# Kernel tuning notes

Measured on AMD Instinct MI355X. Metric: run time of the kernel, lower is better.

Reference implementation:

```python
import jax, jax.numpy as jnp
import numpy as np
from jax import lax


def conv2d(x, w, b=None, pad=0):
    out = lax.conv_general_dilated(x, w, (1, 1), [(pad, pad), (pad, pad)],
                                   dimension_numbers=('NCHW', 'OIHW', 'NCHW'))
    return out if b is None else out + b[None, :, None, None]


def bn_inf(x, gamma, beta, mean, var, eps=1e-5):
    inv = gamma / jnp.sqrt(var + eps)
    return x * inv[None, :, None, None] + (beta - mean * inv)[None, :, None, None]


def silu(x):
    return x * jax.nn.sigmoid(x)


def deform_conv2d(x, offset, weight, groups):
    # torchvision DeformConv2d v1 semantics: kernel 3x3, stride 1, pad 1, dilation 1,
    # one offset group; offset channels interleaved (dy, dx) per kernel tap, row-major taps.
    B, C, H, W = x.shape
    K = 9
    off = offset.reshape(B, K, 2, H, W)
    dy, dx = off[:, :, 0], off[:, :, 1]                      # (B,K,H,W)
    ki = (jnp.arange(K) // 3 - 1).astype(x.dtype)            # kernel row offset (pad=1)
    kj = (jnp.arange(K) % 3 - 1).astype(x.dtype)
    py = jnp.arange(H, dtype=x.dtype)[None, None, :, None] + ki[None, :, None, None] + dy
    px = jnp.arange(W, dtype=x.dtype)[None, None, None, :] + kj[None, :, None, None] + dx
    y0 = jnp.floor(py)
    x0 = jnp.floor(px)
    wy1 = py - y0                                            # bilinear weights
    wx1 = px - x0
    y0i = y0.astype(jnp.int32)
    x0i = x0.astype(jnp.int32)
    xf = x.reshape(B, C, H * W)

    def gather(yi, xi):
        valid = ((yi >= 0) & (yi < H) & (xi >= 0) & (xi < W)).astype(x.dtype)
        idx = (jnp.clip(yi, 0, H - 1) * W + jnp.clip(xi, 0, W - 1)).reshape(B, K * H * W)
        v = jax.vmap(lambda f, i: jnp.take(f, i, axis=-1))(xf, idx).reshape(B, C, K, H, W)
        return v * valid[:, None]

    cols = (gather(y0i, x0i) * ((1 - wy1) * (1 - wx1))[:, None]
            + gather(y0i, x0i + 1) * ((1 - wy1) * wx1)[:, None]
            + gather(y0i + 1, x0i) * (wy1 * (1 - wx1))[:, None]
            + gather(y0i + 1, x0i + 1) * (wy1 * wx1)[:, None])   # (B,C,K,H,W)

    G = groups
    Cg = C // G
    Co = weight.shape[0]
    cols = cols.reshape(B, G, Cg, K, H, W)
    wg = weight.reshape(G, Co // G, Cg, K)
    return jnp.einsum('bgckhw,gock->bgohw', cols, wg).reshape(B, Co, H, W)


def d_clem_forward(x, x_prev, w_off, b_off, w_def, w_cross, w_g1, b_g1,
                   g1_gamma, g1_beta, g1_mean, g1_var, w_g2, b_g2,
                   w_out, b_out, o_gamma, o_beta, o_mean, o_var):
    offset = conv2d(x, w_off, b_off, pad=1)
    x_dir = deform_conv2d(x, offset, w_def, groups=4)
    x_dense = conv2d(jnp.concatenate([x_dir, x_prev], axis=1), w_cross, None, pad=0)
    a = silu(bn_inf(conv2d(x_dense, w_g1, b_g1, pad=1), g1_gamma, g1_beta, g1_mean, g1_var))
    attn = jax.nn.sigmoid(conv2d(a, w_g2, b_g2, pad=0))
    out = silu(bn_inf(conv2d(x_dense * attn, w_out, b_out, pad=0), o_gamma, o_beta, o_mean, o_var))
    return x + out  # use_residual: in_channels == out_channels


def setup_inputs() -> dict:
    key = jax.random.key(0)
    ks = jax.random.split(key, 16)
    B, C, H, W, G = 4, 256, 64, 64, 4

    def wt(k, shape, fan_in):
        return jax.random.normal(k, shape, jnp.float32) / np.float32(np.sqrt(fan_in))

    return {
        'x': jax.random.normal(ks[0], (B, C, H, W), jnp.float32),
        'x_prev': jax.random.normal(ks[1], (B, C, H, W), jnp.float32),
        'w_off': wt(ks[2], (18, C, 3, 3), C * 9),
        'b_off': 0.01 * jax.random.normal(ks[3], (18,), jnp.float32),
        'w_def': wt(ks[4], (C, C // G, 3, 3), (C // G) * 9),
        'w_cross': wt(ks[5], (C, 2 * C, 1, 1), 2 * C),
        'w_g1': wt(ks[6], (C // 4, C, 3, 3), C * 9),
        'b_g1': 0.01 * jax.random.normal(ks[7], (C // 4,), jnp.float32),
        'g1_gamma': 1.0 + 0.1 * jax.random.normal(ks[8], (C // 4,), jnp.float32),
        'g1_beta': 0.1 * jax.random.normal(ks[9], (C // 4,), jnp.float32),
        'g1_mean': 0.1 * jax.random.normal(ks[10], (C // 4,), jnp.float32),
        'g1_var': 0.5 + jax.random.uniform(ks[11], (C // 4,), jnp.float32),
        'w_g2': wt(ks[12], (C, C // 4, 1, 1), C // 4),
        'b_g2': jnp.zeros((C,), jnp.float32),
        'w_out': wt(ks[13], (C, C, 1, 1), C),
        'b_out': jnp.zeros((C,), jnp.float32),
        'o_gamma': 1.0 + 0.1 * jax.random.normal(ks[14], (C,), jnp.float32),
        'o_beta': jnp.zeros((C,), jnp.float32),
        'o_mean': 0.1 * jax.random.normal(ks[15], (C,), jnp.float32),
        'o_var': 0.5 + jax.random.uniform(jax.random.fold_in(key, 99), (C,), jnp.float32),
    }


def reference(x, x_prev, w_off, b_off, w_def, w_cross, w_g1, b_g1,
              g1_gamma, g1_beta, g1_mean, g1_var, w_g2, b_g2,
              w_out, b_out, o_gamma, o_beta, o_mean, o_var):
    return d_clem_forward(x, x_prev, w_off, b_off, w_def, w_cross, w_g1, b_g1,
                          g1_gamma, g1_beta, g1_mean, g1_var, w_g2, b_g2,
                          w_out, b_out, o_gamma, o_beta, o_mean, o_var)
```

## Files before the change

### kernel.cpp

```cpp
#include <hip/hip_runtime.h>
#include <hip/hip_bf16.h>

using bf16 = __hip_bfloat16;
typedef __attribute__((ext_vector_type(8))) short short8;
typedef __attribute__((ext_vector_type(4))) float f32x4;

__device__ __forceinline__ float b2f(bf16 v){ return __bfloat162float(v); }
__device__ __forceinline__ float sigf(float v){ return 1.f/(1.f + __expf(-v)); }
__device__ __forceinline__ float ldv(const float* p, int i){ return p[i]; }
__device__ __forceinline__ float ldv(const bf16* p, int i){ return b2f(p[i]); }
__device__ __forceinline__ void stv(float* p, int i, float v){ p[i] = v; }
__device__ __forceinline__ void stv(bf16* p, int i, float v){ p[i] = __float2bfloat16(v); }
__device__ __forceinline__ float bfe(short8 v, int j){
  unsigned short s = (unsigned short)v[j];
  return b2f(*(bf16*)&s);
}

__device__ __forceinline__ void ld2v(const float* p, float& a, float& b){
  float2 v = *(const float2*)p; a = v.x; b = v.y;
}
__device__ __forceinline__ void ld2v(const bf16* p, float& a, float& b){
  unsigned int u = *(const unsigned int*)p;
  unsigned short s0 = (unsigned short)(u & 0xFFFF), s1 = (unsigned short)(u >> 16);
  a = b2f(*(bf16*)&s0); b = b2f(*(bf16*)&s1);
}
__device__ __forceinline__ void ld8(const bf16* s, unsigned int* pk){
  short8 v = *(const short8*)s;
  #pragma unroll
  for (int e = 0; e < 4; e++)
    pk[e] = (unsigned int)(unsigned short)v[2*e]
          | ((unsigned int)(unsigned short)v[2*e+1] << 16);
}
__device__ __forceinline__ void ld8(const float* s, unsigned int* pk){
  f32x4 a = *(const f32x4*)s, c = *(const f32x4*)(s + 4);
  float vals[8] = {a[0],a[1],a[2],a[3],c[0],c[1],c[2],c[3]};
  #pragma unroll
  for (int e = 0; e < 4; e++){
    bf16 h0 = __float2bfloat16(vals[2*e]), h1 = __float2bfloat16(vals[2*e+1]);
    pk[e] = (unsigned int)*(unsigned short*)&h0
          | ((unsigned int)*(unsigned short*)&h1 << 16);
  }
}

__global__ __launch_bounds__(256) void k_detect(const unsigned short* xs, int* flag){
  __shared__ int cnt;
  if (threadIdx.x == 0) cnt = 0;
  __syncthreads();
  int local = 0;
  for (int i = threadIdx.x; i < 16384; i += 256){
    if (((xs[i] >> 7) & 0xFF) == 0xFF) local++;
  }
  if (local) atomicAdd(&cnt, local);
  __syncthreads();
  if (threadIdx.x == 0) *flag = (cnt > 0) ? 1 : 0;
}

struct ParamSrc { const void* p[18]; };

__global__ __launch_bounds__(256) void k_convert(ParamSrc ps, const int* flagp,
    float* cpar, bf16* wdefb, bf16* woffb, bf16* wg1b, bf16* wcrossb, bf16* woutb,
    float* cwT){
  static constexpr int n[24]   = {41472,18,147456,131072,147456,64,64,64,64,64,
                                  16384,256,65536,256,256,256,256,256,
                                  147456,73728,147456,131072,65536,16384};
  static constexpr int off[18] = {0,41472,41504,188960,320032,467488,467552,467616,
                                  467680,467744,467808,484192,484448,549984,550240,
                                  550496,550752,551008};
  const int s = blockIdx.y;
  const bool f32 = (*flagp != 0);
  if (s == 23){
    for (int i = blockIdx.x * 256 + threadIdx.x; i < 16384; i += gridDim.x * 256){
      const int c = i >> 8, co = i & 255;
      if (f32) cwT[i] = ((const float*)ps.p[10])[co * 64 + c];
      else     cwT[i] = b2f(((const bf16*)ps.p[10])[co * 64 + c]);
    }
    return;
  }
  if (s >= 18){
    static constexpr int srcs[5] = {2, 0, 4, 3, 12};
    const int src_slot = srcs[s - 18];
    bf16* dst = (s == 18) ? wdefb : (s == 19) ? woffb : (s == 20) ? wg1b
              : (s == 21) ? wcrossb : woutb;
    const int nsrc = (s == 19) ? 41472 : n[s];
    const bool remap = (s == 19 || s == 20);
    for (int i = blockIdx.x * 256 + threadIdx.x; i < n[s]; i += gridDim.x * 256){
      int srcIdx = i;
      if (remap){
        const int co = i / 2304, rem = i % 2304;
        const int chunk = rem / 288, r2 = rem % 288;
        const int tap = r2 >> 5, cl = r2 & 31;
        srcIdx = co * 2304 + (chunk * 32 + cl) * 9 + tap;
      }
      if (f32){
        const float* src = (const float*)ps.p[src_slot];
        dst[i] = (srcIdx < nsrc) ? __float2bfloat16(src[srcIdx]) : __float2bfloat16(0.f);
      } else {
        const bf16* src = (const bf16*)ps.p[src_slot];
        dst[i] = (srcIdx < nsrc) ? src[srcIdx] : __float2bfloat16(0.f);
      }
    }
    return;
  }
  float* dst = cpar + off[s];
  if (f32){
    const float* src = (const float*)ps.p[s];
    for (int i = blockIdx.x * 256 + threadIdx.x; i < n[s]; i += gridDim.x * 256)
      dst[i] = src[i];
  } else {
    const bf16* src = (const bf16*)ps.p[s];
    for (int i = blockIdx.x * 256 + threadIdx.x; i < n[s]; i += gridDim.x * 256)
      dst[i] = b2f(src[i]);
  }
}

template<typename T>
__device__ __forceinline__ void xt_body(const T* __restrict__ x, bf16* __restrict__ xt){
  __shared__ float lds[64][65];
  const int bx = blockIdx.x;
  const int b = bx >> 8, y = (bx >> 2) & 63, g = bx & 3;
  const int t = threadIdx.x;
  const int px = t & 63, cq = t >> 6;
  #pragma unroll
  for (int it = 0; it < 16; it++){
    const int ch = cq * 16 + it;
    lds[ch][px] = ldv(x, ((b * 256 + g * 64 + ch) * 64 + y) * 64 + px);
  }
  __syncthreads();
  const int ch = t & 63, pb = t >> 6;
  bf16* ob = xt + ((b * 4 + g) * 4096 + y * 64) * 64 + ch;
  #pragma unroll
  for (int i = 0; i < 16; i++){
    const int p = pb * 16 + i;
    ob[p * 64] = __float2bfloat16(lds[ch][p]);
  }
}

__global__ __launch_bounds__(256) void k_xt(const void* x, const int* flagp, bf16* xt){
  if (*flagp) xt_body((const float*)x, xt);
  else        xt_body((const bf16*)x, xt);
}

template<typename T, int COT>
__device__ __forceinline__ void conv3_raw(const T* __restrict__ xin,
    const bf16* __restrict__ wb, float* __restrict__ outp, int co_lim,
    unsigned short* xt16, int cc_begin){
  const int bx = blockIdx.x;
  const int b = bx >> 6, y = bx & 63;
  const int t = threadIdx.x;
  const int l = t & 63, w = t >> 6;
  const int lm = l & 15, lq = l >> 4;
  const int px = w * 16 + lm;
  f32x4 acc[COT];
  #pragma unroll
  for (int m = 0; m < COT; m++) acc[m] = (f32x4){0.f,0.f,0.f,0.f};

  #pragma unroll
  for (int ch_i = 0; ch_i < 2; ch_i++){
    const int cc = cc_begin + ch_i * 32;
    __syncthreads();
    if (t < 96){
      const int c = t / 3, r = t - c * 3;
      xt16[c * 210 + r * 70 + 3]  = 0;
      xt16[c * 210 + r * 70 + 68] = 0;
    }
    #pragma unroll
    for (int it = 0; it < 3; it++){
      const int u = t + it * 256;
      const int pb = u & 7;
      const int cr = u >> 3;
      const int c = cr / 3, r = cr - c * 3;
      const int yy = y + r - 1;
      const int px0 = pb * 8;
      unsigned int pk[4];
      if ((unsigned)yy < 64u){
        ld8(xin + (b * 256 + cc + c) * 4096 + yy * 64 + px0, pk);
      } else {
        pk[0] = pk[1] = pk[2] = pk[3] = 0;
      }
      unsigned int* dp = (unsigned int*)(xt16 + c * 210 + r * 70 + 4 + px0);
      dp[0] = pk[0]; dp[1] = pk[1]; dp[2] = pk[2]; dp[3] = pk[3];
    }
    __syncthreads();
    const int chunkG = cc >> 5;
    const unsigned short* bt = xt16 + 3 + px;
    #pragma unroll
    for (int tap = 0; tap < 9; tap++){
      const int ti = tap / 3, tj = tap - ti * 3;
      short8 bfr;
      #pragma unroll
      for (int j = 0; j < 8; j++)
        bfr[j] = (short)bt[(lq * 8 + j) * 210 + ti * 70 + tj];
      #pragma unroll
      for (int m = 0; m < COT; m++){
        const bf16* ap = wb + (m * 16 + lm) * 2304 + chunkG * 288 + tap * 32 + lq * 8;
        short8 afr = *(const short8*)ap;
        acc[m] = __builtin_amdgcn_mfma_f32_16x16x32_bf16(afr, bfr, acc[m], 0, 0, 0);
      }
    }
  }
  const int p = y * 64 + px;
  #pragma unroll
  for (int m = 0; m < COT; m++){
    #pragma unroll
    for (int r = 0; r < 4; r++){
      const int co = m * 16 + lq * 4 + r;
      if (co >= co_lim) continue;
      outp[(b * co_lim + co) * 4096 + p] = acc[m][r];
    }
  }
}

__global__ __launch_bounds__(256) void k_coff_m(const void* x, const int* flagp,
    const bf16* woffb, float* offp){
  __shared__ __align__(16) unsigned short xtile[32 * 210];
  float* op = offp + blockIdx.y * 294912;
  const int cc0 = blockIdx.y * 64;
  if (*flagp) conv3_raw<float, 2>((const float*)x, woffb, op, 18, xtile, cc0);
  else        conv3_raw<bf16, 2>((const bf16*)x, woffb, op, 18, xtile, cc0);
}

__global__ __launch_bounds__(256) void k_g1_m(const bf16* xdense,
    const bf16* wg1b, float* abp){
  __shared__ __align__(16) unsigned short xtile[32 * 210];
  float* op = abp + blockIdx.y * 1048576;
  conv3_raw<bf16, 4>(xdense, wg1b, op, 64, xtile, blockIdx.y * 64);
}

__global__ __launch_bounds__(256) void k_omerge(const float* __restrict__ offp,
    const float* __restrict__ cb, float* __restrict__ offc){
  const int i4 = (blockIdx.x * 256 + threadIdx.x) * 4;
  constexpr int PS = 294912;
  f32x4 a = *(const f32x4*)(offp + i4);
  f32x4 b = *(const f32x4*)(offp + PS + i4);
  f32x4 c = *(const f32x4*)(offp + 2 * PS + i4);
  f32x4 d = *(const f32x4*)(offp + 3 * PS + i4);
  const int co = (i4 >> 12) % 18;
  const float bias = cb[co];
  f32x4 r;
  #pragma unroll
  for (int j = 0; j < 4; j++) r[j] = ((a[j] + b[j]) + c[j]) + d[j] + bias;
  *(f32x4*)(offc + i4) = r;
}

#define CROWM 600

__global__ __launch_bounds__(256) void k_deform(const bf16* __restrict__ xt,
    const float* __restrict__ offc, const bf16* __restrict__ wdefb,
    bf16* __restrict__ xdir){
  __shared__ __align__(16) unsigned short cols[32 * CROWM];
  const int g = blockIdx.y;
  const int q0 = blockIdx.x * 32;
  const int b = q0 >> 12, p0 = q0 & 4095;
  const int t = threadIdx.x;
  {
    const int pos = t & 31, u8 = t >> 5;
    const int c0 = u8 * 8;
    const int p = p0 + pos;
    const int y = p >> 6, xx = p & 63;
    const float* ob = offc + b * 18 * 4096 + p;
    const bf16* xg = xt + (b * 4 + g) * 4096 * 64;
    #pragma unroll
    for (int k = 0; k < 9; k++){
      float dy = ob[(2 * k) * 4096];
      float dx = ob[(2 * k + 1) * 4096];
      float py = (float)(y + k / 3 - 1) + dy;
      float px = (float)(xx + k % 3 - 1) + dx;
      float y0f = floorf(py), x0f = floorf(px);
      int y0 = (int)y0f, x0 = (int)x0f;
      float wy1 = py - y0f, wx1 = px - x0f;
      float wy0 = 1.f - wy1, wx0 = 1.f - wx1;
      bool vy0 = (unsigned)y0 < 64u, vy1 = (unsigned)(y0 + 1) < 64u;
      bool vx0 = (unsigned)x0 < 64u, vx1 = (unsigned)(x0 + 1) < 64u;
      float w00 = (vy0 && vx0) ? wy0 * wx0 : 0.f;
      float w01 = (vy0 && vx1) ? wy0 * wx1 : 0.f;
      float w10 = (vy1 && vx0) ? wy1 * wx0 : 0.f;
      float w11 = (vy1 && vx1) ? wy1 * wx1 : 0.f;
      int yc0 = min(max(y0, 0), 63), yc1 = min(max(y0 + 1, 0), 63);
      int xc0 = min(max(x0, 0), 63), xc1 = min(max(x0 + 1, 0), 63);
      int i00 = yc0 * 64 + xc0, i01 = yc0 * 64 + xc1;
      int i10 = yc1 * 64 + xc0, i11 = yc1 * 64 + xc1;
      short8 s00 = *(const short8*)(xg + i00 * 64 + c0);
      short8 s01 = *(const short8*)(xg + i01 * 64 + c0);
      short8 s10 = *(const short8*)(xg + i10 * 64 + c0);
      short8 s11 = *(const short8*)(xg + i11 * 64 + c0);
      #pragma unroll
      for (int j = 0; j < 8; j++){
        float val = w00 * bfe(s00, j) + w01 * bfe(s01, j)
                  + w10 * bfe(s10, j) + w11 * bfe(s11, j);
        bf16 hv = __float2bfloat16(val);
        cols[pos * CROWM + (c0 + j) * 9 + k] = *(unsigned short*)&hv;
      }
    }
  }
  __syncthreads();
  {
    const int w = t >> 6;
    const int l = t & 63;
    const int lrow = l & 15;
    const int lhi = l >> 4;
    f32x4 acc0 = {0.f, 0.f, 0.f, 0.f};
    f32x4 acc1 = {0.f, 0.f, 0.f, 0.f};
    const bf16* wr = wdefb + (g * 64 + w * 16 + lrow) * 576;
    const unsigned short* b0p = cols + lrow * CROWM;
    const unsigned short* b1p = cols + (16 + lrow) * CROWM;
    #pragma unroll 2
    for (int kk = 0; kk < 576; kk += 32){
      int ko = kk + lhi * 8;
      short8 a  = *(const short8*)(wr + ko);
      short8 b0 = *(const short8*)(b0p + ko);
      short8 b1 = *(const short8*)(b1p + ko);
      acc0 = __builtin_amdgcn_mfma_f32_16x16x32_bf16(a, b0, acc0, 0, 0, 0);
      acc1 = __builtin_amdgcn_mfma_f32_16x16x32_bf16(a, b1, acc1, 0, 0, 0);
    }
    const int co_base = g * 64 + w * 16 + lhi * 4;
    #pragma unroll
    for (int r = 0; r < 4; r++){
      bf16* xo = xdir + (b * 256 + co_base + r) * 4096 + p0 + lrow;
      xo[0]  = __float2bfloat16(acc0[r]);
      xo[16] = __float2bfloat16(acc1[r]);
    }
  }
}

template<typename T>
__device__ __forceinline__ void cross_mfma_body(const bf16* __restrict__ xdir,
    const T* __restrict__ xprev, const bf16* __restrict__ wb,
    bf16* __restrict__ xdense, unsigned short* cols){
  const int bx = blockIdx.x;
  const int b = bx >> 6, y = bx & 63;
  const int co0 = blockIdx.y * 128;
  const int t = threadIdx.x;
  const int l = t & 63, w = t >> 6;
  const int lm = l & 15, lq = l >> 4;
  const int pos2 = t & 31, cq = t >> 5;
  unsigned int* cols32 = (unsigned int*)cols;
  f32x4 acc[8];
  #pragma unroll
  for (int m = 0; m < 8; m++) acc[m] = (f32x4){0.f,0.f,0.f,0.f};

  for (int cc = 0; cc < 512; cc += 64){
    __syncthreads();
    #pragma unroll
    for (int c8 = 0; c8 < 8; c8++){
      const int cl = cq * 8 + c8;
      const int ci = cc + cl;
      float v0, v1;
      if (ci < 256) ld2v(xdir + (b * 256 + ci) * 4096 + y * 64 + 2 * pos2, v0, v1);
      else          ld2v(xprev + (b * 256 + (ci - 256)) * 4096 + y * 64 + 2 * pos2, v0, v1);
      bf16 h0 = __float2bfloat16(v0), h1 = __float2bfloat16(v1);
      unsigned int packed = (unsigned int)*(unsigned short*)&h0
                          | ((unsigned int)*(unsigned short*)&h1 << 16);
      cols32[cl * 34 + pos2] = packed;
    }
    __syncthreads();
    #pragma unroll
    for (int kk = 0; kk < 64; kk += 32){
      short8 bfr;
      #pragma unroll
      for (int j = 0; j < 8; j++)
        bfr[j] = (short)cols[(kk + lq * 8 + j) * 68 + w * 16 + lm];
      #pragma unroll
      for (int m = 0; m < 8; m++){
        const bf16* ap = wb + (co0 + m * 16 + lm) * 512 + cc + kk + lq * 8;
        short8 afr = *(const short8*)ap;
        acc[m] = __builtin_amdgcn_mfma_f32_16x16x32_bf16(afr, bfr, acc[m], 0, 0, 0);
      }
    }
  }
  const int p = y * 64 + w * 16 + lm;
  #pragma unroll
  for (int m = 0; m < 8; m++){
    #pragma unroll
    for (int r = 0; r < 4; r++){
      const int co = co0 + m * 16 + lq * 4 + r;
      xdense[(b * 256 + co) * 4096 + p] = __float2bfloat16(acc[m][r]);
    }
  }
}

__global__ __launch_bounds__(256) void k_cross(const bf16* xdir, const void* xprev,
    const int* flagp, const bf16* wcb, bf16* xdense){
  __shared__ __align__(16) unsigned short cols[64 * 68];
  if (*flagp) cross_mfma_body(xdir, (const float*)xprev, wcb, xdense, cols);
  else        cross_mfma_body(xdir, (const bf16*)xprev, wcb, xdense, cols);
}

__global__ __launch_bounds__(256) void k_attn(const float* __restrict__ abp,
    const float* __restrict__ cb1, const float* __restrict__ gam,
    const float* __restrict__ bet, const float* __restrict__ mea,
    const float* __restrict__ var, const float* __restrict__ cwT,
    const float* __restrict__ cb2, const bf16* __restrict__ xdense,
    bf16* __restrict__ xa){
  __shared__ float a_s[64][17];
  const int bx = blockIdx.x;
  const int b = bx >> 8, pc = bx & 255;
  const int p0 = pc * 16;
  const int t = threadIdx.x;
  constexpr int PS = 1048576;
  {
    const int ch = t >> 2;
    const int px0 = (t & 3) * 4;
    const float inv = gam[ch] * rsqrtf(var[ch] + 1e-5f);
    const float sh  = bet[ch] - mea[ch] * inv;
    const float bias = cb1[ch];
    const int ai = (b * 64 + ch) * 4096 + p0 + px0;
    #pragma unroll
    for (int j = 0; j < 4; j++){
      float s = ((abp[ai + j] + abp[PS + ai + j]) + abp[2 * PS + ai + j])
              + abp[3 * PS + ai + j];
      s += bias;
      s = s * inv + sh;
      s = s * sigf(s);
      a_s[ch][px0 + j] = s;
    }
  }
  __syncthreads();
  const int co = t;
  float acc[16];
  #pragma unroll
  for (int i = 0; i < 16; i++) acc[i] = 0.f;
  for (int c = 0; c < 64; c++){
    const float wv = cwT[c * 256 + co];
    #pragma unroll
    for (int i = 0; i < 16; i++) acc[i] += wv * a_s[c][i];
  }
  const float bias2 = cb2[co];
  const int base = (b * 256 + co) * 4096 + p0;
  #pragma unroll
  for (int i = 0; i < 16; i++){
    float attn = sigf(acc[i] + bias2);
    xa[base + i] = __float2bfloat16(b2f(xdense[base + i]) * attn);
  }
}

template<typename T>
__device__ __forceinline__ void out_mfma_body(const bf16* __restrict__ xa,
    const bf16* __restrict__ wb, const float* __restrict__ cbv,
    const float* __restrict__ gam, const float* __restrict__ bet,
    const float* __restrict__ mea, const float* __restrict__ var,
    const T* __restrict__ xres, T* __restrict__ outp, unsigned short* cols){
  const int bx = blockIdx.x;
  const int b = bx >> 6, y = bx & 63;
  const int co0 = blockIdx.y * 128;
  const int t = threadIdx.x;
  const int l = t & 63, w = t >> 6;
  const int lm = l & 15, lq = l >> 4;
  const int pos2 = t & 31, cq = t >> 5;
  unsigned int* cols32 = (unsigned int*)cols;
  f32x4 acc[8];
  #pragma unroll
  for (int m = 0; m < 8; m++) acc[m] = (f32x4){0.f,0.f,0.f,0.f};

  for (int cc = 0; cc < 256; cc += 64){
    __syncthreads();
    #pragma unroll
    for (int c8 = 0; c8 < 8; c8++){
      const int cl = cq * 8 + c8;
      const int ci = cc + cl;
      const unsigned int u = *(const unsigned int*)(xa + (b * 256 + ci) * 4096
                                                    + y * 64 + 2 * pos2);
      cols32[cl * 34 + pos2] = u;
    }
    __syncthreads();
    #pragma unroll
    for (int kk = 0; kk < 64; kk += 32){
      short8 bfr;
      #pragma unroll
      for (int j = 0; j < 8; j++)
        bfr[j] = (short)cols[(kk + lq * 8 + j) * 68 + w * 16 + lm];
      #pragma unroll
      for (int m = 0; m < 8; m++){
        const bf16* ap = wb + (co0 + m * 16 + lm) * 256 + cc + kk + lq * 8;
        short8 afr = *(const short8*)ap;
        acc[m] = __builtin_amdgcn_mfma_f32_16x16x32_bf16(afr, bfr, acc[m], 0, 0, 0);
      }
    }
  }
  const int p = y * 64 + w * 16 + lm;
  #pragma unroll
  for (int m = 0; m < 8; m++){
    #pragma unroll
    for (int r = 0; r < 4; r++){
      const int co = co0 + m * 16 + lq * 4 + r;
      float inv = gam[co] * rsqrtf(var[co] + 1e-5f);
      float v = acc[m][r] + cbv[co];
      v = v * inv + (bet[co] - mea[co] * inv);
      v = v * sigf(v);
      const int idx = (b * 256 + co) * 4096 + p;
      stv(outp, idx, v + ldv(xres, idx));
    }
  }
}

__global__ __launch_bounds__(256) void k_out(const bf16* xa, const bf16* wob,
    const float* cb, const float* gam, const float* bet, const float* mea,
    const float* var, const void* xres, void* out, const int* flagp){
  __shared__ __align__(16) unsigned short cols[64 * 68];
  if (*flagp) out_mfma_body(xa, wob, cb, gam, bet, mea, var,
                            (const float*)xres, (float*)out, cols);
  else        out_mfma_body(xa, wob, cb, gam, bet, mea, var,
                            (const bf16*)xres, (bf16*)out, cols);
}

extern "C" void kernel_launch(void* const* d_in, const int* in_sizes, int n_in,
                              void* d_out, int out_size, void* d_ws, size_t ws_size,
                              hipStream_t stream) {
  const void* x      = d_in[0];
  const void* x_prev = d_in[1];

  float* ws   = (float*)d_ws;
  int*   flag = (int*)ws;
  float* cpar = ws + 16;
  float* cb_off   = cpar + 41472;
  float* cb_g1    = cpar + 467488;
  float* cg1_gam  = cpar + 467552;
  float* cg1_bet  = cpar + 467616;
  float* cg1_mea  = cpar + 467680;
  float* cg1_var  = cpar + 467744;
  float* cb_g2    = cpar + 484192;
  float* cb_out   = cpar + 549984;
  float* co_gam   = cpar + 550240;
  float* co_bet   = cpar + 550496;
  float* co_mea   = cpar + 550752;
  float* co_var   = cpar + 551008;

  float* cwT     = ws + 16 + 551264;
  bf16*  wdefb   = (bf16*)(ws + 567664);
  bf16*  woffb   = (bf16*)(ws + 641392);
  bf16*  wg1b    = (bf16*)(ws + 678256);
  bf16*  wcrossb = (bf16*)(ws + 751984);
  bf16*  woutb   = (bf16*)(ws + 817520);
  float* base    = ws + 850288;
  float* offp    = base;
  float* offc    = offp + 1179648;
  float* abp     = offc + 294912;
  bf16*  xdirb   = (bf16*)(abp + 4194304);
  bf16*  xdenseb = (bf16*)(abp + 6291456);
  bf16*  xtb     = (bf16*)(abp + 8388608);
  bf16*  xab     = xdirb;

  ParamSrc ps;
  for (int i = 0; i < 18; i++) ps.p[i] = d_in[2 + i];

  k_detect<<<dim3(1), 256, 0, stream>>>((const unsigned short*)x, flag);
  k_convert<<<dim3(96, 24), 256, 0, stream>>>(ps, flag, cpar, wdefb, woffb,
                                              wg1b, wcrossb, woutb, cwT);
  k_xt<<<dim3(1024), 256, 0, stream>>>(x, flag, xtb);
  k_coff_m<<<dim3(256, 4), 256, 0, stream>>>(x, flag, woffb, offp);
  k_omerge<<<dim3(288), 256, 0, stream>>>(offp, cb_off, offc);
  k_deform<<<dim3(512, 4), 256, 0, stream>>>(xtb, offc, wdefb, xdirb);
  k_cross<<<dim3(256, 2), 256, 0, stream>>>(xdirb, x_prev, flag, wcrossb, xdenseb);
  k_g1_m<<<dim3(256, 4), 256, 0, stream>>>(xdenseb, wg1b, abp);
  k_attn<<<dim3(1024), 256, 0, stream>>>(abp, cb_g1, cg1_gam, cg1_bet, cg1_mea,
                                         cg1_var, cwT, cb_g2, xdenseb, xab);
  k_out<<<dim3(256, 2), 256, 0, stream>>>(xab, woutb, cb_out, co_gam, co_bet,
                                          co_mea, co_var, x, d_out, flag);
}
```

Measured before the change: 349.9 us.

## Prefetch next channel tile into registers and halve output-channel tile in cross/out GEMMs

The cross and out 1x1-conv MFMA kernels now load the next 64-channel activation slice into registers while the current slice is consumed from shared memory, so global loads overlap with the MFMA work. The output-channel tile per block drops from 128 to 64 and the grid doubles, which raises block count and occupancy. The xdir path in the cross kernel also loads packed bf16 directly instead of converting through float. In exchange, each activation tile is now staged twice as many times across blocks, and each thread holds more registers for the prefetch buffer.

```diff
diff --git a/kernel.cpp b/kernel.cpp
--- a/kernel.cpp
+++ b/kernel.cpp
@@ -323,36 +323,50 @@
 }
 
 template<typename T>
+__device__ __forceinline__ void cross_load(const bf16* __restrict__ xdir,
+    const T* __restrict__ xprev, int b, int y, int pos2, int cq, int cc,
+    unsigned int* pk){
+  #pragma unroll
+  for (int c8 = 0; c8 < 8; c8++){
+    const int ci = cc + cq * 8 + c8;
+    if (ci < 256){
+      pk[c8] = *(const unsigned int*)(xdir + (b * 256 + ci) * 4096 + y * 64 + 2 * pos2);
+    } else {
+      float v0, v1;
+      ld2v(xprev + (b * 256 + (ci - 256)) * 4096 + y * 64 + 2 * pos2, v0, v1);
+      bf16 h0 = __float2bfloat16(v0), h1 = __float2bfloat16(v1);
+      pk[c8] = (unsigned int)*(unsigned short*)&h0
+             | ((unsigned int)*(unsigned short*)&h1 << 16);
+    }
+  }
+}
+
+template<typename T>
 __device__ __forceinline__ void cross_mfma_body(const bf16* __restrict__ xdir,
     const T* __restrict__ xprev, const bf16* __restrict__ wb,
     bf16* __restrict__ xdense, unsigned short* cols){
   const int bx = blockIdx.x;
   const int b = bx >> 6, y = bx & 63;
-  const int co0 = blockIdx.y * 128;
+  const int co0 = blockIdx.y * 64;
   const int t = threadIdx.x;
   const int l = t & 63, w = t >> 6;
   const int lm = l & 15, lq = l >> 4;
   const int pos2 = t & 31, cq = t >> 5;
   unsigned int* cols32 = (unsigned int*)cols;
-  f32x4 acc[8];
-  #pragma unroll
-  for (int m = 0; m < 8; m++) acc[m] = (f32x4){0.f,0.f,0.f,0.f};
-
-  for (int cc = 0; cc < 512; cc += 64){
+  f32x4 acc[4];
+  #pragma unroll
+  for (int m = 0; m < 4; m++) acc[m] = (f32x4){0.f,0.f,0.f,0.f};
+  unsigned int pk[8];
+  cross_load(xdir, xprev, b, y, pos2, cq, 0, pk);
+
+  for (int c = 0; c < 8; c++){
     __syncthreads();
     #pragma unroll
-    for (int c8 = 0; c8 < 8; c8++){
-      const int cl = cq * 8 + c8;
-      const int ci = cc + cl;
-      float v0, v1;
-      if (ci < 256) ld2v(xdir + (b * 256 + ci) * 4096 + y * 64 + 2 * pos2, v0, v1);
-      else          ld2v(xprev + (b * 256 + (ci - 256)) * 4096 + y * 64 + 2 * pos2, v0, v1);
-      bf16 h0 = __float2bfloat16(v0), h1 = __float2bfloat16(v1);
-      unsigned int packed = (unsigned int)*(unsigned short*)&h0
-                          | ((unsigned int)*(unsigned short*)&h1 << 16);
-      cols32[cl * 34 + pos2] = packed;
-    }
+    for (int c8 = 0; c8 < 8; c8++)
+      cols32[(cq * 8 + c8) * 34 + pos2] = pk[c8];
     __syncthreads();
+    if (c < 7) cross_load(xdir, xprev, b, y, pos2, cq, (c + 1) * 64, pk);
+    const int cc = c * 64;
     #pragma unroll
     for (int kk = 0; kk < 64; kk += 32){
       short8 bfr;
@@ -360,7 +374,7 @@
       for (int j = 0; j < 8; j++)
         bfr[j] = (short)cols[(kk + lq * 8 + j) * 68 + w * 16 + lm];
       #pragma unroll
-      for (int m = 0; m < 8; m++){
+      for (int m = 0; m < 4; m++){
         const bf16* ap = wb + (co0 + m * 16 + lm) * 512 + cc + kk + lq * 8;
         short8 afr = *(const short8*)ap;
         acc[m] = __builtin_amdgcn_mfma_f32_16x16x32_bf16(afr, bfr, acc[m], 0, 0, 0);
@@ -369,7 +383,7 @@
   }
   const int p = y * 64 + w * 16 + lm;
   #pragma unroll
-  for (int m = 0; m < 8; m++){
+  for (int m = 0; m < 4; m++){
     #pragma unroll
     for (int r = 0; r < 4; r++){
       const int co = co0 + m * 16 + lq * 4 + r;
@@ -433,6 +447,15 @@
   }
 }
 
+__device__ __forceinline__ void out_load(const bf16* __restrict__ xa,
+    int b, int y, int pos2, int cq, int cc, unsigned int* pk){
+  #pragma unroll
+  for (int c8 = 0; c8 < 8; c8++){
+    const int ci = cc + cq * 8 + c8;
+    pk[c8] = *(const unsigned int*)(xa + (b * 256 + ci) * 4096 + y * 64 + 2 * pos2);
+  }
+}
+
 template<typename T>
 __device__ __forceinline__ void out_mfma_body(const bf16* __restrict__ xa,
     const bf16* __restrict__ wb, const float* __restrict__ cbv,
@@ -441,27 +464,26 @@
     const T* __restrict__ xres, T* __restrict__ outp, unsigned short* cols){
   const int bx = blockIdx.x;
   const int b = bx >> 6, y = bx & 63;
-  const int co0 = blockIdx.y * 128;
+  const int co0 = blockIdx.y * 64;
   const int t = threadIdx.x;
   const int l = t & 63, w = t >> 6;
   const int lm = l & 15, lq = l >> 4;
   const int pos2 = t & 31, cq = t >> 5;
   unsigned int* cols32 = (unsigned int*)cols;
-  f32x4 acc[8];
-  #pragma unroll
-  for (int m = 0; m < 8; m++) acc[m] = (f32x4){0.f,0.f,0.f,0.f};
-
-  for (int cc = 0; cc < 256; cc += 64){
+  f32x4 acc[4];
+  #pragma unroll
+  for (int m = 0; m < 4; m++) acc[m] = (f32x4){0.f,0.f,0.f,0.f};
+  unsigned int pk[8];
+  out_load(xa, b, y, pos2, cq, 0, pk);
+
+  for (int c = 0; c < 4; c++){
     __syncthreads();
     #pragma unroll
-    for (int c8 = 0; c8 < 8; c8++){
-      const int cl = cq * 8 + c8;
-      const int ci = cc + cl;
-      const unsigned int u = *(const unsigned int*)(xa + (b * 256 + ci) * 4096
-                                                    + y * 64 + 2 * pos2);
-      cols32[cl * 34 + pos2] = u;
-    }
+    for (int c8 = 0; c8 < 8; c8++)
+      cols32[(cq * 8 + c8) * 34 + pos2] = pk[c8];
     __syncthreads();
+    if (c < 3) out_load(xa, b, y, pos2, cq, (c + 1) * 64, pk);
+    const int cc = c * 64;
     #pragma unroll
     for (int kk = 0; kk < 64; kk += 32){
       short8 bfr;
@@ -469,7 +491,7 @@
       for (int j = 0; j < 8; j++)
         bfr[j] = (short)cols[(kk + lq * 8 + j) * 68 + w * 16 + lm];
       #pragma unroll
-      for (int m = 0; m < 8; m++){
+      for (int m = 0; m < 4; m++){
         const bf16* ap = wb + (co0 + m * 16 + lm) * 256 + cc + kk + lq * 8;
         short8 afr = *(const short8*)ap;
         acc[m] = __builtin_amdgcn_mfma_f32_16x16x32_bf16(afr, bfr, acc[m], 0, 0, 0);
@@ -478,7 +500,7 @@
   }
   const int p = y * 64 + w * 16 + lm;
   #pragma unroll
-  for (int m = 0; m < 8; m++){
+  for (int m = 0; m < 4; m++){
     #pragma unroll
     for (int r = 0; r < 4; r++){
       const int co = co0 + m * 16 + lq * 4 + r;
@@ -549,10 +571,10 @@
   k_coff_m<<<dim3(256, 4), 256, 0, stream>>>(x, flag, woffb, offp);
   k_omerge<<<dim3(288), 256, 0, stream>>>(offp, cb_off, offc);
   k_deform<<<dim3(512, 4), 256, 0, stream>>>(xtb, offc, wdefb, xdirb);
-  k_cross<<<dim3(256, 2), 256, 0, stream>>>(xdirb, x_prev, flag, wcrossb, xdenseb);
+  k_cross<<<dim3(256, 4), 256, 0, stream>>>(xdirb, x_prev, flag, wcrossb, xdenseb);
   k_g1_m<<<dim3(256, 4), 256, 0, stream>>>(xdenseb, wg1b, abp);
   k_attn<<<dim3(1024), 256, 0, stream>>>(abp, cb_g1, cg1_gam, cg1_bet, cg1_mea,
                                          cg1_var, cwT, cb_g2, xdenseb, xab);
-  k_out<<<dim3(256, 2), 256, 0, stream>>>(xab, woutb, cb_out, co_gam, co_bet,
+  k_out<<<dim3(256, 4), 256, 0, stream>>>(xab, woutb, cb_out, co_gam, co_bet,
                                           co_mea, co_var, x, d_out, flag);
 }
```

Result: faster. 328.5 us (-6.1%).
